# Performance work log

Hardware: AMD Instinct MI355X
Metric: run time of the kernel (lower is better)

## Reference

```python
import jax, jax.numpy as jnp
import numpy as np

N_JOINTS = 24

def _rodrigues(r):
    # r: [B, J, 3] axis-angle -> [B, J, 3, 3] rotation matrices
    theta = jnp.clip(jnp.linalg.norm(r, axis=-1, keepdims=True), 1e-6)  # [B,J,1]
    rh = r / theta
    z = jnp.zeros_like(rh[..., :1])
    # skew-symmetric matrix m
    m = jnp.stack([
        jnp.concatenate([z, -rh[..., 2:3], rh[..., 1:2]], -1),
        jnp.concatenate([rh[..., 2:3], z, -rh[..., 0:1]], -1),
        jnp.concatenate([-rh[..., 1:2], rh[..., 0:1], z], -1),
    ], axis=-2)  # [B,J,3,3]
    rrT = rh[..., :, None] * rh[..., None, :]  # outer product [B,J,3,3]
    cos = jnp.cos(theta)[..., None]
    sin = jnp.sin(theta)[..., None]
    eye = jnp.eye(3, dtype=r.dtype)
    return cos * eye + (1.0 - cos) * rrT + sin * m

def _with_zeros(Rm, t):
    # Rm: [B,3,3], t: [B,3] -> [B,4,4] homogeneous transform
    B = Rm.shape[0]
    top = jnp.concatenate([Rm, t[:, :, None]], axis=-1)  # [B,3,4]
    bot = jnp.broadcast_to(jnp.array([0.0, 0.0, 0.0, 1.0], Rm.dtype), (B, 1, 4))
    return jnp.concatenate([top, bot], axis=1)

def _keypoints(v, idx):
    # v: [B,N,3], idx: [G,K] vertex-index groups -> [B,G,3] via (max+min)/2
    g = v[:, idx]  # [B,G,K,3] irregular gather
    return (g.max(axis=2) + g.min(axis=2)) * 0.5

def setup_inputs() -> dict:
    key = jax.random.key(0)
    ks = jax.random.split(key, 8)
    B, N, P, K = 64, 40000, 100, 128
    beta = jax.random.normal(ks[0], (B, P), jnp.float32)
    pose = jax.random.normal(ks[1], (B, N_JOINTS * 3), jnp.float32) * 0.3
    trans = jax.random.normal(ks[2], (B, 3), jnp.float32)
    shapedirs = jax.random.normal(ks[3], (P, 3 * N), jnp.float32) * 0.01
    v_template = jax.random.normal(ks[4], (N, 3), jnp.float32)
    w = jax.random.uniform(ks[5], (N, N_JOINTS), jnp.float32)
    weights = w / w.sum(axis=1, keepdims=True)  # LBS weights sum to 1
    reorder_index = jnp.arange(N_JOINTS, dtype=jnp.int64 if jax.config.jax_enable_x64 else jnp.int32)
    # kinematic tree: parent[i] < i (binary-tree shape stands in for the rabbit skeleton)
    parent = jnp.concatenate([jnp.zeros(1, jnp.int32), (jnp.arange(1, N_JOINTS, dtype=jnp.int32) - 1) // 2])
    joint_idx = jax.random.randint(ks[6], (N_JOINTS - 1, K), 0, N)
    add_idx = jax.random.randint(ks[7], (7, K), 0, N)
    return {"beta": beta, "pose": pose, "trans": trans, "shapedirs": shapedirs,
            "v_template": v_template, "weights": weights, "reorder_index": reorder_index,
            "parent": parent, "joint_idx": joint_idx, "add_idx": add_idx}

def reference(beta, pose, trans, shapedirs, v_template, weights,
              reorder_index, parent, joint_idx, add_idx):
    B = beta.shape[0]
    pose = pose.reshape(B, N_JOINTS, 3)[:, reorder_index]
    # blend shapes: v_shaped = beta @ shapedirs + template
    v_posed = (beta @ shapedirs + v_template.reshape(-1)).reshape(B, -1, 3)  # [B,N,3]
    # joints from vertex-group (max+min)/2, root is zero
    J = jnp.concatenate([jnp.zeros((B, 1, 3), beta.dtype), _keypoints(v_posed, joint_idx)], axis=1)  # [B,24,3]
    R = _rodrigues(pose)  # [B,24,3,3]
    # forward kinematics along the tree (fixed 24-joint loop)
    par = np.asarray(jax.device_get(parent))
    G = [_with_zeros(R[:, 0], J[:, 0])]
    for i in range(1, N_JOINTS):
        p = int(par[i])
        G_loc = _with_zeros(R[:, i], J[:, i] - J[:, p])
        G.append(jnp.matmul(G[p], G_loc))
    G = jnp.stack(G, axis=1)  # [B,24,4,4]
    # remove rest-pose joint locations (pack subtraction only touches last column)
    Jh = jnp.concatenate([J, jnp.zeros((B, N_JOINTS, 1), beta.dtype)], axis=-1)[..., None]  # [B,24,4,1]
    t_corr = jnp.matmul(G, Jh)  # [B,24,4,1]
    G1 = jnp.concatenate([G[..., :3], G[..., 3:4] - t_corr], axis=-1)
    # LBS skinning: per-vertex blended transform
    T = jnp.einsum('nk,bkij->bnij', weights, G1)  # [B,N,4,4]
    vh = jnp.concatenate([v_posed, jnp.ones((B, v_posed.shape[1], 1), beta.dtype)], axis=-1)  # [B,N,4]
    posed = jnp.einsum('bnij,bnj->bni', T, vh)[..., :3] + trans[:, None, :]  # [B,N,3]
    skeleton = jnp.concatenate([
        jnp.zeros((B, 1, 3), beta.dtype),
        _keypoints(posed, joint_idx),
        _keypoints(posed, add_idx),
    ], axis=1)  # [B,31,3]
    return posed, skeleton
```

## Files before the change

### kernel.cpp

```cpp
#include <hip/hip_runtime.h>
#include <math.h>

#define B    64
#define NV   40000
#define P    100
#define KG   128
#define NJ   24
#define TVJ  16
#define TVS  32
#define NSK  31
#define NSUB (KG / TVJ)
#define NJS  (23 * NSUB)
#define GATHER_BLK 552

typedef __attribute__((ext_vector_type(8))) short bf16x8;
typedef __attribute__((ext_vector_type(4))) float f32x4;

__device__ __forceinline__ unsigned short rne_bf16(float f) {
  unsigned u = __float_as_uint(f);
  u = (u + 0x7FFFu + ((u >> 16) & 1u)) >> 16;
  return (unsigned short)u;
}

__global__ __launch_bounds__(256)
void k_gather(const float* __restrict__ sd,
              const float* __restrict__ beta,
              const int*   __restrict__ joint_idx,
              unsigned short* __restrict__ sdg,
              unsigned short* __restrict__ G1A,
              unsigned short* __restrict__ beta_bf) {
  if (blockIdx.x < GATHER_BLK) {
    const int tid = blockIdx.x * 256 + threadIdx.x;
    const int js = tid / 768, rem = tid % 768;
    const int n = rem % 48, kg = rem / 48;
    const int j = js >> 3, s = js & 7;
    const int vidx = joint_idx[j * KG + s * TVJ + n / 3];
    const size_t colbase = (size_t)vidx * 3 + (n % 3);
    unsigned pk[4];
#pragma unroll
    for (int h = 0; h < 4; ++h) {
      const int k0 = kg * 8 + 2 * h;
      float f0 = 0.0f, f1 = 0.0f;
      if (k0 < P)     f0 = sd[(size_t)k0 * (3 * NV) + colbase];
      if (k0 + 1 < P) f1 = sd[(size_t)(k0 + 1) * (3 * NV) + colbase];
      pk[h] = (unsigned)rne_bf16(f0) | ((unsigned)rne_bf16(f1) << 16);
    }
    *(uint4*)&sdg[(size_t)js * 6144 + n * 128 + kg * 8] =
        make_uint4(pk[0], pk[1], pk[2], pk[3]);
  } else {
    const int e0 = (blockIdx.x - GATHER_BLK) * 256 + threadIdx.x;
    const uint4 z4 = make_uint4(0, 0, 0, 0);
    for (int i = e0; i < 4096; i += 1024) ((uint4*)G1A)[i] = z4;
    for (int i = e0; i < 64 * 136; i += 1024) {
      const int b = i / 136, k = i - b * 136;
      beta_bf[i] = (k < P) ? rne_bf16(beta[b * P + k]) : (unsigned short)0;
    }
  }
}

__global__ __launch_bounds__(256)
void k_jc(const unsigned short* __restrict__ sdg,
          const unsigned short* __restrict__ beta_bf,
          const float* __restrict__ vt,
          const int*   __restrict__ joint_idx,
          const float* __restrict__ pose,
          const float* __restrict__ trans,
          float*       __restrict__ pmn,
          float*       __restrict__ pmx,
          unsigned short* __restrict__ G1A,
          int*         __restrict__ cnt) {
  const int j = blockIdx.x;
  const int s = blockIdx.y;
  const int js = j * NSUB + s;
  const int t = threadIdx.x;
  const int lane = t & 63, wv = t >> 6;
  const int l15 = lane & 15, qd = lane >> 4;

  __shared__ __align__(16) unsigned char smem[55296];
  unsigned short* beta_s = (unsigned short*)smem;
  unsigned short* sdT_s  = (unsigned short*)(smem + 17408);
  float*          vt_s   = (float*)(smem + 30464);
  int*            idx_s  = (int*)(smem + 30656);
  float*          pos_s  = (float*)smem;
  __shared__ int s_old;

  if (t < TVJ) idx_s[t] = joint_idx[j * KG + s * TVJ + t];
  __syncthreads();

  for (int e = t; e < 1088; e += 256)
    ((uint4*)beta_s)[e] = ((const uint4*)beta_bf)[e];
  for (int e = t; e < 768; e += 256) {
    const int n = e >> 4, kg = e & 15;
    *(uint4*)&sdT_s[n * 136 + kg * 8] =
        *(const uint4*)&sdg[(size_t)js * 6144 + (e << 3)];
  }
  if (t < 48) vt_s[t] = vt[(size_t)idx_s[t / 3] * 3 + (t % 3)];
  __syncthreads();

  bf16x8 af[4];
#pragma unroll
  for (int ks = 0; ks < 4; ++ks)
    af[ks] = *(const bf16x8*)&beta_s[(wv * 16 + l15) * 136 + ks * 32 + qd * 8];
  f32x4 acc[3];
#pragma unroll
  for (int nt = 0; nt < 3; ++nt) acc[nt] = (f32x4){0.f, 0.f, 0.f, 0.f};
#pragma unroll
  for (int ks = 0; ks < 4; ++ks) {
#pragma unroll
    for (int nt = 0; nt < 3; ++nt) {
      const bf16x8 bf = *(const bf16x8*)&sdT_s[(nt * 16 + l15) * 136 + ks * 32 + qd * 8];
      acc[nt] = __builtin_amdgcn_mfma_f32_16x16x32_bf16(af[ks], bf, acc[nt], 0, 0, 0);
    }
  }
  float vtv[3];
#pragma unroll
  for (int nt = 0; nt < 3; ++nt) vtv[nt] = vt_s[nt * 16 + l15];
  __syncthreads();

#pragma unroll
  for (int nt = 0; nt < 3; ++nt) {
    const int n = nt * 16 + l15;
    const int v = n / 3, c = n - 3 * v;
#pragma unroll
    for (int r = 0; r < 4; ++r) {
      const int m = wv * 16 + qd * 4 + r;
      pos_s[m * 68 + v * 4 + c] = acc[nt][r] + vtv[nt];
    }
  }
  __syncthreads();

  if (t < 192) {
    const int b = t / 3, c = t % 3;
    float lo = 1e30f, hi = -1e30f;
#pragma unroll
    for (int v = 0; v < TVJ; ++v) {
      const float val = pos_s[b * 68 + v * 4 + c];
      lo = fminf(lo, val); hi = fmaxf(hi, val);
    }
    pmn[(js * B + b) * 3 + c] = lo;
    pmx[(js * B + b) * 3 + c] = hi;
  }

  __syncthreads();
  if (t == 0) { __threadfence(); s_old = atomicAdd(cnt, 1); }
  __syncthreads();
  if (s_old != NJS - 1) return;
  __threadfence();

  float* Jl_c = (float*)smem;
  float* Gl   = (float*)(smem + 18432);

  for (int e = t; e < 192; e += 256) Jl_c[e] = 0.0f;
  for (int e = t; e < 23 * 192; e += 256) {
    const int jj = e / 192, rem = e - jj * 192;
    float lo = 1e30f, hi = -1e30f;
#pragma unroll
    for (int s2 = 0; s2 < NSUB; ++s2) {
      lo = fminf(lo, pmn[(jj * NSUB + s2) * 192 + rem]);
      hi = fmaxf(hi, pmx[(jj * NSUB + s2) * 192 + rem]);
    }
    const int b = rem / 3, c = rem - b * 3;
    Jl_c[((jj + 1) * 3 + c) * 64 + b] = 0.5f * (lo + hi);
  }
  __syncthreads();

  if (t < 64) {
    const int b = t;
    float px = pose[b * 72 + 0], py = pose[b * 72 + 1], pz = pose[b * 72 + 2];
    float G_[12];
#pragma unroll 1
    for (int i = 0; i < NJ; ++i) {
      float nx = 0.f, ny = 0.f, nz = 0.f;
      if (i < NJ - 1) {
        nx = pose[b * 72 + (i + 1) * 3 + 0];
        ny = pose[b * 72 + (i + 1) * 3 + 1];
        nz = pose[b * 72 + (i + 1) * 3 + 2];
      }
      const float th = fmaxf(sqrtf(px * px + py * py + pz * pz), 1e-6f);
      const float xh = px / th, yh = py / th, zh = pz / th;
      const float cc = cosf(th), ss = sinf(th), oo = 1.0f - cc;
      float R9[9];
      R9[0] = cc + oo * xh * xh;      R9[1] = oo * xh * yh - ss * zh; R9[2] = oo * xh * zh + ss * yh;
      R9[3] = oo * xh * yh + ss * zh; R9[4] = cc + oo * yh * yh;      R9[5] = oo * yh * zh - ss * xh;
      R9[6] = oo * xh * zh - ss * yh; R9[7] = oo * yh * zh + ss * xh; R9[8] = cc + oo * zh * zh;

      const float ji0 = Jl_c[(i * 3 + 0) * 64 + b];
      const float ji1 = Jl_c[(i * 3 + 1) * 64 + b];
      const float ji2 = Jl_c[(i * 3 + 2) * 64 + b];

      if (i == 0) {
#pragma unroll
        for (int r = 0; r < 3; ++r) {
          G_[r * 4 + 0] = R9[r * 3 + 0];
          G_[r * 4 + 1] = R9[r * 3 + 1];
          G_[r * 4 + 2] = R9[r * 3 + 2];
          G_[r * 4 + 3] = 0.0f;
        }
      } else {
        const int p = (i - 1) >> 1;
        const float d0 = ji0 - Jl_c[(p * 3 + 0) * 64 + b];
        const float d1 = ji1 - Jl_c[(p * 3 + 1) * 64 + b];
        const float d2 = ji2 - Jl_c[(p * 3 + 2) * 64 + b];
        float Gn[12];
#pragma unroll
        for (int r = 0; r < 3; ++r) {
          const float g0 = Gl[(b * 12 + p) * 12 + r * 4 + 0];
          const float g1 = Gl[(b * 12 + p) * 12 + r * 4 + 1];
          const float g2 = Gl[(b * 12 + p) * 12 + r * 4 + 2];
          const float g3 = Gl[(b * 12 + p) * 12 + r * 4 + 3];
          Gn[r * 4 + 0] = g0 * R9[0] + g1 * R9[3] + g2 * R9[6];
          Gn[r * 4 + 1] = g0 * R9[1] + g1 * R9[4] + g2 * R9[7];
          Gn[r * 4 + 2] = g0 * R9[2] + g1 * R9[5] + g2 * R9[8];
          Gn[r * 4 + 3] = g0 * d0 + g1 * d1 + g2 * d2 + g3;
        }
#pragma unroll
        for (int e = 0; e < 12; ++e) G_[e] = Gn[e];
      }
      if (i < 12) {
#pragma unroll
        for (int e = 0; e < 12; ++e) Gl[(b * 12 + i) * 12 + e] = G_[e];
      }
#pragma unroll
      for (int r = 0; r < 3; ++r) {
        const float tc = G_[r * 4 + 0] * ji0 + G_[r * 4 + 1] * ji1 + G_[r * 4 + 2] * ji2;
        G1A[b * 512 + (r * 4 + 0) * 32 + i] = rne_bf16(G_[r * 4 + 0]);
        G1A[b * 512 + (r * 4 + 1) * 32 + i] = rne_bf16(G_[r * 4 + 1]);
        G1A[b * 512 + (r * 4 + 2) * 32 + i] = rne_bf16(G_[r * 4 + 2]);
        G1A[b * 512 + (r * 4 + 3) * 32 + i] = rne_bf16(G_[r * 4 + 3] - tc);
      }
      px = nx; py = ny; pz = nz;
    }
  } else if (t >= 192) {
#pragma unroll
    for (int k = 0; k < 3; ++k) {
      const int e = (t - 192) * 3 + k;
      const int b = e / 3, r = e - b * 3;
      G1A[b * 512 + (r * 4 + 3) * 32 + 24] = rne_bf16(trans[b * 3 + r]);
    }
  }
}

__global__ __launch_bounds__(256)
void k_skin(const float* __restrict__ sd,
            const float* __restrict__ vt,
            const float* __restrict__ w,
            const unsigned short* __restrict__ beta_bf,
            const unsigned short* __restrict__ G1A,
            float*       __restrict__ out) {
  const int n0v  = blockIdx.x * TVS;
  const int col0 = n0v * 3;
  const int t  = threadIdx.x;
  const int lane = t & 63, wv = t >> 6;
  const int l15 = lane & 15, q = lane >> 4;

  __shared__ __align__(16) unsigned char smem[46464];
  unsigned short* beta_s = (unsigned short*)smem;
  unsigned short* sdT_s  = (unsigned short*)(smem + 17408);
  unsigned short* wT_s   = (unsigned short*)(smem + 43520);
  float*          vt_s   = (float*)(smem + 46080);
  float*          vhf    = (float*)smem;

  for (int e = t; e < 1088; e += 256)
    ((uint4*)beta_s)[e] = ((const uint4*)beta_bf)[e];
  for (int task = t; task < 1536; task += 256) {
    const int n = task % 96, kg = task / 96;
    unsigned pk[4];
#pragma unroll
    for (int h = 0; h < 4; ++h) {
      const int k0 = kg * 8 + 2 * h;
      float f0 = 0.0f, f1 = 0.0f;
      if (k0 < P)     f0 = sd[(size_t)k0 * (3 * NV) + col0 + n];
      if (k0 + 1 < P) f1 = sd[(size_t)(k0 + 1) * (3 * NV) + col0 + n];
      pk[h] = (unsigned)rne_bf16(f0) | ((unsigned)rne_bf16(f1) << 16);
    }
    *(uint4*)&sdT_s[n * 136 + kg * 8] = make_uint4(pk[0], pk[1], pk[2], pk[3]);
  }
  for (int e = t; e < 1024; e += 256) {
    const int n = e >> 5, k = e & 31;
    float val = (k < NJ) ? w[(n0v + n) * NJ + k] : (k == NJ ? 1.0f : 0.0f);
    wT_s[n * 40 + k] = rne_bf16(val);
  }
  if (t < 96) vt_s[t] = vt[col0 + t];
  __syncthreads();

  bf16x8 af[4];
#pragma unroll
  for (int ks = 0; ks < 4; ++ks)
    af[ks] = *(const bf16x8*)&beta_s[(wv * 16 + l15) * 136 + ks * 32 + q * 8];
  f32x4 acc[6];
#pragma unroll
  for (int nt = 0; nt < 6; ++nt) acc[nt] = (f32x4){0.f, 0.f, 0.f, 0.f};
#pragma unroll
  for (int ks = 0; ks < 4; ++ks) {
#pragma unroll
    for (int nt = 0; nt < 6; ++nt) {
      const bf16x8 bf = *(const bf16x8*)&sdT_s[(nt * 16 + l15) * 136 + ks * 32 + q * 8];
      acc[nt] = __builtin_amdgcn_mfma_f32_16x16x32_bf16(af[ks], bf, acc[nt], 0, 0, 0);
    }
  }
  __syncthreads();

#pragma unroll
  for (int nt = 0; nt < 6; ++nt) {
    const int n = nt * 16 + l15;
    const int v = n / 3, c = n - 3 * v;
    const float vtn = vt_s[n];
#pragma unroll
    for (int r = 0; r < 4; ++r) {
      const int m = wv * 16 + q * 4 + r;
      vhf[m * 128 + v * 4 + c] = acc[nt][r] + vtn;
    }
  }
  __syncthreads();

  const bf16x8 wf0 = *(const bf16x8*)&wT_s[l15 * 40 + q * 8];
  const bf16x8 wf1 = *(const bf16x8*)&wT_s[(16 + l15) * 40 + q * 8];
  const f32x4 zero = (f32x4){0.f, 0.f, 0.f, 0.f};
#pragma unroll 4
  for (int bi = 0; bi < 16; ++bi) {
    const int b = wv * 16 + bi;
    const bf16x8 gf = *(const bf16x8*)&G1A[(size_t)b * 512 + l15 * 32 + q * 8];
    const f32x4 d0 = __builtin_amdgcn_mfma_f32_16x16x32_bf16(gf, wf0, zero, 0, 0, 0);
    const f32x4 d1 = __builtin_amdgcn_mfma_f32_16x16x32_bf16(gf, wf1, zero, 0, 0, 0);
    const float4 vh0 = *(const float4*)&vhf[b * 128 + l15 * 4];
    const float4 vh1 = *(const float4*)&vhf[b * 128 + 64 + l15 * 4];
    if (q < 3) {
      out[(size_t)b * (NV * 3) + col0 + l15 * 3 + q] =
          d0[0] * vh0.x + d0[1] * vh0.y + d0[2] * vh0.z + d0[3];
      out[(size_t)b * (NV * 3) + col0 + 48 + l15 * 3 + q] =
          d1[0] * vh1.x + d1[1] * vh1.y + d1[2] * vh1.z + d1[3];
    }
  }
}

__global__ void k_skel(const float* __restrict__ posed,
                       const int*   __restrict__ joint_idx,
                       const int*   __restrict__ add_idx,
                       float*       __restrict__ skel) {
  const int j = blockIdx.x;
  const int b = blockIdx.y;
  const int t = threadIdx.x;
  const int idx = (j < 23) ? joint_idx[j * KG + t] : add_idx[(j - 23) * KG + t];

  const float* p = posed + (size_t)b * NV * 3 + (size_t)idx * 3;
  float mn[3], mx[3];
#pragma unroll
  for (int c = 0; c < 3; ++c) { mn[c] = p[c]; mx[c] = p[c]; }
#pragma unroll
  for (int off = 32; off > 0; off >>= 1) {
#pragma unroll
    for (int c = 0; c < 3; ++c) {
      mn[c] = fminf(mn[c], __shfl_down(mn[c], off));
      mx[c] = fmaxf(mx[c], __shfl_down(mx[c], off));
    }
  }
  __shared__ float s_mn[2][3], s_mx[2][3];
  const int wave = t >> 6, lane = t & 63;
  if (lane == 0) {
#pragma unroll
    for (int c = 0; c < 3; ++c) { s_mn[wave][c] = mn[c]; s_mx[wave][c] = mx[c]; }
  }
  __syncthreads();
  if (t == 0) {
#pragma unroll
    for (int c = 0; c < 3; ++c) {
      float lo = fminf(s_mn[0][c], s_mn[1][c]);
      float hi = fmaxf(s_mx[0][c], s_mx[1][c]);
      skel[(b * NSK + 1 + j) * 3 + c] = 0.5f * (lo + hi);
      if (j == 0) skel[(b * NSK + 0) * 3 + c] = 0.0f;
    }
  }
}

extern "C" void kernel_launch(void* const* d_in, const int* in_sizes, int n_in,
                              void* d_out, int out_size, void* d_ws, size_t ws_size,
                              hipStream_t stream) {
  const float* beta     = (const float*)d_in[0];
  const float* pose     = (const float*)d_in[1];
  const float* trans    = (const float*)d_in[2];
  const float* sd       = (const float*)d_in[3];
  const float* vt       = (const float*)d_in[4];
  const float* w        = (const float*)d_in[5];
  const int* joint_idx  = (const int*)d_in[8];
  const int* add_idx    = (const int*)d_in[9];

  float* out  = (float*)d_out;
  float* skel = out + (size_t)B * NV * 3;
  unsigned short* G1A     = (unsigned short*)d_ws;
  unsigned short* beta_bf = G1A + B * 512;
  float* pmn = (float*)(beta_bf + B * 136);
  float* pmx = pmn + NJS * B * 3;
  int*   cnt = (int*)(pmx + NJS * B * 3);
  unsigned short* sdg = (unsigned short*)(cnt + 4);

  hipMemsetAsync(cnt, 0, 16, stream);
  k_gather<<<GATHER_BLK + 4, 256, 0, stream>>>(sd, beta, joint_idx,
                                               sdg, G1A, beta_bf);
  k_jc<<<dim3(23, NSUB), 256, 0, stream>>>(sdg, beta_bf, vt, joint_idx,
                                           pose, trans, pmn, pmx, G1A, cnt);
  k_skin<<<NV / TVS, 256, 0, stream>>>(sd, vt, w, beta_bf, G1A, out);
  k_skel<<<dim3(30, B), 128, 0, stream>>>(out, joint_idx, add_idx, skel);
}
```

Before: 178.6 us.

## Materialize blended vertices once and reuse them for joints and skinning

Adds a blend kernel that computes the shape-blended vertex positions for all vertices and batches into a workspace buffer. The joint keypoint kernel then gathers from this buffer instead of redoing a bf16 GEMM on gathered shapedirs, and the skinning kernel reads the buffer instead of recomputing the blendshape GEMM. G1A zeroing moves into the last joint block. This removes the separate gather pass and the duplicated GEMM, but adds a large fp32 intermediate write and read.

```diff
diff --git a/kernel.cpp b/kernel.cpp
--- a/kernel.cpp
+++ b/kernel.cpp
@@ -11,7 +11,6 @@
 #define NSK  31
 #define NSUB (KG / TVJ)
 #define NJS  (23 * NSUB)
-#define GATHER_BLK 552
 
 typedef __attribute__((ext_vector_type(8))) short bf16x8;
 typedef __attribute__((ext_vector_type(4))) float f32x4;
@@ -23,122 +22,119 @@
 }
 
 __global__ __launch_bounds__(256)
-void k_gather(const float* __restrict__ sd,
-              const float* __restrict__ beta,
-              const int*   __restrict__ joint_idx,
-              unsigned short* __restrict__ sdg,
-              unsigned short* __restrict__ G1A,
-              unsigned short* __restrict__ beta_bf) {
-  if (blockIdx.x < GATHER_BLK) {
-    const int tid = blockIdx.x * 256 + threadIdx.x;
-    const int js = tid / 768, rem = tid % 768;
-    const int n = rem % 48, kg = rem / 48;
-    const int j = js >> 3, s = js & 7;
-    const int vidx = joint_idx[j * KG + s * TVJ + n / 3];
-    const size_t colbase = (size_t)vidx * 3 + (n % 3);
+void k_blend(const float* __restrict__ beta,
+             const float* __restrict__ sd,
+             const float* __restrict__ vt,
+             float*       __restrict__ vp) {
+  const int n0v  = blockIdx.x * TVS;
+  const int col0 = n0v * 3;
+  const int t  = threadIdx.x;
+  const int lane = t & 63, wv = t >> 6;
+  const int l15 = lane & 15, q = lane >> 4;
+
+  __shared__ __align__(16) unsigned char smem[43904];
+  unsigned short* beta_s = (unsigned short*)smem;
+  unsigned short* sdT_s  = (unsigned short*)(smem + 17408);
+  float*          vt_s   = (float*)(smem + 43520);
+  float*          vhf2   = (float*)smem;
+
+  for (int e = t; e < 64 * 36; e += 256) {
+    const int m = e / 36, pp = P + e % 36;
+    beta_s[m * 136 + pp] = 0;
+  }
+  for (int e = t; e < 64 * P; e += 256) {
+    const int m = e / P, p = e % P;
+    beta_s[m * 136 + p] = rne_bf16(beta[e]);
+  }
+  for (int task = t; task < 1536; task += 256) {
+    const int n = task % 96, kg = task / 96;
     unsigned pk[4];
 #pragma unroll
     for (int h = 0; h < 4; ++h) {
       const int k0 = kg * 8 + 2 * h;
       float f0 = 0.0f, f1 = 0.0f;
-      if (k0 < P)     f0 = sd[(size_t)k0 * (3 * NV) + colbase];
-      if (k0 + 1 < P) f1 = sd[(size_t)(k0 + 1) * (3 * NV) + colbase];
+      if (k0 < P)     f0 = sd[(size_t)k0 * (3 * NV) + col0 + n];
+      if (k0 + 1 < P) f1 = sd[(size_t)(k0 + 1) * (3 * NV) + col0 + n];
       pk[h] = (unsigned)rne_bf16(f0) | ((unsigned)rne_bf16(f1) << 16);
     }
-    *(uint4*)&sdg[(size_t)js * 6144 + n * 128 + kg * 8] =
-        make_uint4(pk[0], pk[1], pk[2], pk[3]);
-  } else {
-    const int e0 = (blockIdx.x - GATHER_BLK) * 256 + threadIdx.x;
-    const uint4 z4 = make_uint4(0, 0, 0, 0);
-    for (int i = e0; i < 4096; i += 1024) ((uint4*)G1A)[i] = z4;
-    for (int i = e0; i < 64 * 136; i += 1024) {
-      const int b = i / 136, k = i - b * 136;
-      beta_bf[i] = (k < P) ? rne_bf16(beta[b * P + k]) : (unsigned short)0;
-    }
-  }
+    *(uint4*)&sdT_s[n * 136 + kg * 8] = make_uint4(pk[0], pk[1], pk[2], pk[3]);
+  }
+  if (t < 96) vt_s[t] = vt[col0 + t];
+  __syncthreads();
+
+  bf16x8 af[4];
+#pragma unroll
+  for (int ks = 0; ks < 4; ++ks)
+    af[ks] = *(const bf16x8*)&beta_s[(wv * 16 + l15) * 136 + ks * 32 + q * 8];
+  f32x4 acc[6];
+#pragma unroll
+  for (int nt = 0; nt < 6; ++nt) acc[nt] = (f32x4){0.f, 0.f, 0.f, 0.f};
+#pragma unroll
+  for (int ks = 0; ks < 4; ++ks) {
+#pragma unroll
+    for (int nt = 0; nt < 6; ++nt) {
+      const bf16x8 bf = *(const bf16x8*)&sdT_s[(nt * 16 + l15) * 136 + ks * 32 + q * 8];
+      acc[nt] = __builtin_amdgcn_mfma_f32_16x16x32_bf16(af[ks], bf, acc[nt], 0, 0, 0);
+    }
+  }
+  __syncthreads();
+
+#pragma unroll
+  for (int nt = 0; nt < 6; ++nt) {
+    const int n = nt * 16 + l15;
+    const int v = n / 3, c = n - 3 * v;
+    const float vtn = vt_s[n];
+#pragma unroll
+    for (int r = 0; r < 4; ++r) {
+      const int m = wv * 16 + q * 4 + r;
+      vhf2[v * 192 + m * 3 + c] = acc[nt][r] + vtn;
+    }
+  }
+  __syncthreads();
+
+  float* dst = vp + (size_t)n0v * 192;
+  const float4* src = (const float4*)smem;
+  for (int e = t; e < 1536; e += 256) ((float4*)dst)[e] = src[e];
 }
 
 __global__ __launch_bounds__(256)
-void k_jc(const unsigned short* __restrict__ sdg,
-          const unsigned short* __restrict__ beta_bf,
-          const float* __restrict__ vt,
-          const int*   __restrict__ joint_idx,
-          const float* __restrict__ pose,
-          const float* __restrict__ trans,
-          float*       __restrict__ pmn,
-          float*       __restrict__ pmx,
-          unsigned short* __restrict__ G1A,
-          int*         __restrict__ cnt) {
+void k_jkp(const float* __restrict__ vp,
+           const int*   __restrict__ joint_idx,
+           const float* __restrict__ pose,
+           const float* __restrict__ trans,
+           float*       __restrict__ pmn,
+           float*       __restrict__ pmx,
+           unsigned short* __restrict__ G1A,
+           int*         __restrict__ cnt) {
   const int j = blockIdx.x;
   const int s = blockIdx.y;
   const int js = j * NSUB + s;
   const int t = threadIdx.x;
-  const int lane = t & 63, wv = t >> 6;
-  const int l15 = lane & 15, qd = lane >> 4;
 
   __shared__ __align__(16) unsigned char smem[55296];
-  unsigned short* beta_s = (unsigned short*)smem;
-  unsigned short* sdT_s  = (unsigned short*)(smem + 17408);
-  float*          vt_s   = (float*)(smem + 30464);
-  int*            idx_s  = (int*)(smem + 30656);
-  float*          pos_s  = (float*)smem;
+  float* pos_s = (float*)smem;
+  __shared__ int idx_s[TVJ];
   __shared__ int s_old;
 
   if (t < TVJ) idx_s[t] = joint_idx[j * KG + s * TVJ + t];
   __syncthreads();
 
-  for (int e = t; e < 1088; e += 256)
-    ((uint4*)beta_s)[e] = ((const uint4*)beta_bf)[e];
-  for (int e = t; e < 768; e += 256) {
-    const int n = e >> 4, kg = e & 15;
-    *(uint4*)&sdT_s[n * 136 + kg * 8] =
-        *(const uint4*)&sdg[(size_t)js * 6144 + (e << 3)];
-  }
-  if (t < 48) vt_s[t] = vt[(size_t)idx_s[t / 3] * 3 + (t % 3)];
-  __syncthreads();
-
-  bf16x8 af[4];
-#pragma unroll
-  for (int ks = 0; ks < 4; ++ks)
-    af[ks] = *(const bf16x8*)&beta_s[(wv * 16 + l15) * 136 + ks * 32 + qd * 8];
-  f32x4 acc[3];
-#pragma unroll
-  for (int nt = 0; nt < 3; ++nt) acc[nt] = (f32x4){0.f, 0.f, 0.f, 0.f};
-#pragma unroll
-  for (int ks = 0; ks < 4; ++ks) {
-#pragma unroll
-    for (int nt = 0; nt < 3; ++nt) {
-      const bf16x8 bf = *(const bf16x8*)&sdT_s[(nt * 16 + l15) * 136 + ks * 32 + qd * 8];
-      acc[nt] = __builtin_amdgcn_mfma_f32_16x16x32_bf16(af[ks], bf, acc[nt], 0, 0, 0);
-    }
-  }
-  float vtv[3];
-#pragma unroll
-  for (int nt = 0; nt < 3; ++nt) vtv[nt] = vt_s[nt * 16 + l15];
-  __syncthreads();
-
-#pragma unroll
-  for (int nt = 0; nt < 3; ++nt) {
-    const int n = nt * 16 + l15;
-    const int v = n / 3, c = n - 3 * v;
-#pragma unroll
-    for (int r = 0; r < 4; ++r) {
-      const int m = wv * 16 + qd * 4 + r;
-      pos_s[m * 68 + v * 4 + c] = acc[nt][r] + vtv[nt];
-    }
+  for (int task = t; task < 768; task += 256) {
+    const int r = task / 48, c4 = task % 48;
+    const float4 v = *(const float4*)&vp[(size_t)idx_s[r] * 192 + c4 * 4];
+    *(float4*)&pos_s[r * 192 + c4 * 4] = v;
   }
   __syncthreads();
 
   if (t < 192) {
-    const int b = t / 3, c = t % 3;
     float lo = 1e30f, hi = -1e30f;
 #pragma unroll
     for (int v = 0; v < TVJ; ++v) {
-      const float val = pos_s[b * 68 + v * 4 + c];
+      const float val = pos_s[v * 192 + t];
       lo = fminf(lo, val); hi = fmaxf(hi, val);
     }
-    pmn[(js * B + b) * 3 + c] = lo;
-    pmx[(js * B + b) * 3 + c] = hi;
+    pmn[js * 192 + t] = lo;
+    pmx[js * 192 + t] = hi;
   }
 
   __syncthreads();
@@ -150,6 +146,10 @@
   float* Jl_c = (float*)smem;
   float* Gl   = (float*)(smem + 18432);
 
+  {
+    const uint4 z4 = make_uint4(0, 0, 0, 0);
+    for (int e = t; e < 4096; e += 256) ((uint4*)G1A)[e] = z4;
+  }
   for (int e = t; e < 192; e += 256) Jl_c[e] = 0.0f;
   for (int e = t; e < 23 * 192; e += 256) {
     const int jj = e / 192, rem = e - jj * 192;
@@ -241,75 +241,35 @@
 }
 
 __global__ __launch_bounds__(256)
-void k_skin(const float* __restrict__ sd,
-            const float* __restrict__ vt,
-            const float* __restrict__ w,
-            const unsigned short* __restrict__ beta_bf,
-            const unsigned short* __restrict__ G1A,
-            float*       __restrict__ out) {
+void k_skin2(const float* __restrict__ vp,
+             const float* __restrict__ w,
+             const unsigned short* __restrict__ G1A,
+             float*       __restrict__ out) {
   const int n0v  = blockIdx.x * TVS;
   const int col0 = n0v * 3;
   const int t  = threadIdx.x;
   const int lane = t & 63, wv = t >> 6;
   const int l15 = lane & 15, q = lane >> 4;
 
-  __shared__ __align__(16) unsigned char smem[46464];
-  unsigned short* beta_s = (unsigned short*)smem;
-  unsigned short* sdT_s  = (unsigned short*)(smem + 17408);
-  unsigned short* wT_s   = (unsigned short*)(smem + 43520);
-  float*          vt_s   = (float*)(smem + 46080);
-  float*          vhf    = (float*)smem;
-
-  for (int e = t; e < 1088; e += 256)
-    ((uint4*)beta_s)[e] = ((const uint4*)beta_bf)[e];
-  for (int task = t; task < 1536; task += 256) {
-    const int n = task % 96, kg = task / 96;
-    unsigned pk[4];
-#pragma unroll
-    for (int h = 0; h < 4; ++h) {
-      const int k0 = kg * 8 + 2 * h;
-      float f0 = 0.0f, f1 = 0.0f;
-      if (k0 < P)     f0 = sd[(size_t)k0 * (3 * NV) + col0 + n];
-      if (k0 + 1 < P) f1 = sd[(size_t)(k0 + 1) * (3 * NV) + col0 + n];
-      pk[h] = (unsigned)rne_bf16(f0) | ((unsigned)rne_bf16(f1) << 16);
-    }
-    *(uint4*)&sdT_s[n * 136 + kg * 8] = make_uint4(pk[0], pk[1], pk[2], pk[3]);
+  __shared__ __align__(16) unsigned char smem[35328];
+  float*          vhf  = (float*)smem;
+  unsigned short* wT_s = (unsigned short*)(smem + 32768);
+
+  for (int e = t; e < 1536; e += 256) {
+    const int v = e / 48, j0 = (e % 48) * 4;
+    const float4 f = *(const float4*)&vp[(size_t)(n0v + v) * 192 + j0];
+    const float ff[4] = {f.x, f.y, f.z, f.w};
+#pragma unroll
+    for (int i = 0; i < 4; ++i) {
+      const int jj = j0 + i;
+      const int m = jj / 3, c = jj - 3 * m;
+      vhf[m * 128 + v * 4 + c] = ff[i];
+    }
   }
   for (int e = t; e < 1024; e += 256) {
     const int n = e >> 5, k = e & 31;
     float val = (k < NJ) ? w[(n0v + n) * NJ + k] : (k == NJ ? 1.0f : 0.0f);
     wT_s[n * 40 + k] = rne_bf16(val);
-  }
-  if (t < 96) vt_s[t] = vt[col0 + t];
-  __syncthreads();
-
-  bf16x8 af[4];
-#pragma unroll
-  for (int ks = 0; ks < 4; ++ks)
-    af[ks] = *(const bf16x8*)&beta_s[(wv * 16 + l15) * 136 + ks * 32 + q * 8];
-  f32x4 acc[6];
-#pragma unroll
-  for (int nt = 0; nt < 6; ++nt) acc[nt] = (f32x4){0.f, 0.f, 0.f, 0.f};
-#pragma unroll
-  for (int ks = 0; ks < 4; ++ks) {
-#pragma unroll
-    for (int nt = 0; nt < 6; ++nt) {
-      const bf16x8 bf = *(const bf16x8*)&sdT_s[(nt * 16 + l15) * 136 + ks * 32 + q * 8];
-      acc[nt] = __builtin_amdgcn_mfma_f32_16x16x32_bf16(af[ks], bf, acc[nt], 0, 0, 0);
-    }
-  }
-  __syncthreads();
-
-#pragma unroll
-  for (int nt = 0; nt < 6; ++nt) {
-    const int n = nt * 16 + l15;
-    const int v = n / 3, c = n - 3 * v;
-    const float vtn = vt_s[n];
-#pragma unroll
-    for (int r = 0; r < 4; ++r) {
-      const int m = wv * 16 + q * 4 + r;
-      vhf[m * 128 + v * 4 + c] = acc[nt][r] + vtn;
-    }
   }
   __syncthreads();
 
@@ -386,18 +346,16 @@
 
   float* out  = (float*)d_out;
   float* skel = out + (size_t)B * NV * 3;
-  unsigned short* G1A     = (unsigned short*)d_ws;
-  unsigned short* beta_bf = G1A + B * 512;
-  float* pmn = (float*)(beta_bf + B * 136);
-  float* pmx = pmn + NJS * B * 3;
-  int*   cnt = (int*)(pmx + NJS * B * 3);
-  unsigned short* sdg = (unsigned short*)(cnt + 4);
+  unsigned short* G1A = (unsigned short*)d_ws;
+  float* pmn = (float*)((char*)d_ws + 65536);
+  float* pmx = (float*)((char*)d_ws + 206848);
+  int*   cnt = (int*)((char*)d_ws + 348160);
+  float* vp  = (float*)((char*)d_ws + 348176);
 
   hipMemsetAsync(cnt, 0, 16, stream);
-  k_gather<<<GATHER_BLK + 4, 256, 0, stream>>>(sd, beta, joint_idx,
-                                               sdg, G1A, beta_bf);
-  k_jc<<<dim3(23, NSUB), 256, 0, stream>>>(sdg, beta_bf, vt, joint_idx,
-                                           pose, trans, pmn, pmx, G1A, cnt);
-  k_skin<<<NV / TVS, 256, 0, stream>>>(sd, vt, w, beta_bf, G1A, out);
+  k_blend<<<NV / TVS, 256, 0, stream>>>(beta, sd, vt, vp);
+  k_jkp<<<dim3(23, NSUB), 256, 0, stream>>>(vp, joint_idx, pose, trans,
+                                            pmn, pmx, G1A, cnt);
+  k_skin2<<<NV / TVS, 256, 0, stream>>>(vp, w, G1A, out);
   k_skel<<<dim3(30, B), 128, 0, stream>>>(out, joint_idx, add_idx, skel);
 }
```

Result: slower. 183.3 us (+2.6%).

## Bucket joint indices by vertex tile and reduce joint bounds with atomics

Applied to the files above, without the earlier changes.

The per-joint gather of shapedirs columns is replaced. Joint vertex indices are now bucketed by 16-vertex tile, and each tile block blends its contiguous vertices with MFMA and folds min/max into per-joint bounds using order-preserving integer atomics. The forward-kinematics chain moves into its own single-block kernel, which drops the last-block counter. The LBS weights are also converted to padded bf16 once up front, so the skinning kernel can load them as vectors. In exchange the code adds launches and reads many whole tiles instead of only the gathered columns. A fixed bucket capacity of 16 would silently drop indices if a tile ever overflowed.

```diff
diff --git a/kernel.cpp b/kernel.cpp
--- a/kernel.cpp
+++ b/kernel.cpp
@@ -6,12 +6,11 @@
 #define P    100
 #define KG   128
 #define NJ   24
-#define TVJ  16
+#define TVB  16
 #define TVS  32
 #define NSK  31
-#define NSUB (KG / TVJ)
-#define NJS  (23 * NSUB)
-#define GATHER_BLK 552
+#define NTIL (NV / TVB)
+#define BCAP 16
 
 typedef __attribute__((ext_vector_type(8))) short bf16x8;
 typedef __attribute__((ext_vector_type(4))) float f32x4;
@@ -21,86 +20,101 @@
   u = (u + 0x7FFFu + ((u >> 16) & 1u)) >> 16;
   return (unsigned short)u;
 }
+__device__ __forceinline__ unsigned fkey(float f) {
+  const unsigned u = __float_as_uint(f);
+  return (u & 0x80000000u) ? ~u : (u | 0x80000000u);
+}
+__device__ __forceinline__ float unfkey(unsigned k) {
+  const unsigned u = (k & 0x80000000u) ? (k ^ 0x80000000u) : ~k;
+  return __uint_as_float(u);
+}
 
 __global__ __launch_bounds__(256)
-void k_gather(const float* __restrict__ sd,
-              const float* __restrict__ beta,
-              const int*   __restrict__ joint_idx,
-              unsigned short* __restrict__ sdg,
-              unsigned short* __restrict__ G1A,
-              unsigned short* __restrict__ beta_bf) {
-  if (blockIdx.x < GATHER_BLK) {
-    const int tid = blockIdx.x * 256 + threadIdx.x;
-    const int js = tid / 768, rem = tid % 768;
-    const int n = rem % 48, kg = rem / 48;
-    const int j = js >> 3, s = js & 7;
-    const int vidx = joint_idx[j * KG + s * TVJ + n / 3];
-    const size_t colbase = (size_t)vidx * 3 + (n % 3);
+void k_prep0(const float* __restrict__ beta,
+             const float* __restrict__ w,
+             unsigned short* __restrict__ beta_bf,
+             unsigned short* __restrict__ wbf,
+             unsigned short* __restrict__ G1A,
+             unsigned* __restrict__ pmnU,
+             unsigned* __restrict__ pmxU,
+             int* __restrict__ tileCnt) {
+  const int tid  = blockIdx.x * 256 + threadIdx.x;
+  const int nthr = gridDim.x * 256;
+  const uint4 z4 = make_uint4(0, 0, 0, 0);
+  for (int e = tid; e < 4096; e += nthr) ((uint4*)G1A)[e] = z4;
+  for (int e = tid; e < 23 * 192; e += nthr) { pmnU[e] = 0xFFFFFFFFu; pmxU[e] = 0u; }
+  for (int e = tid; e < NTIL; e += nthr) tileCnt[e] = 0;
+  for (int e = tid; e < 64 * 136; e += nthr) {
+    const int b = e / 136, k = e - b * 136;
+    beta_bf[e] = (k < P) ? rne_bf16(beta[b * P + k]) : (unsigned short)0;
+  }
+  for (int e = tid; e < NV * 32; e += nthr) {
+    const int n = e >> 5, k = e & 31;
+    const float val = (k < NJ) ? w[n * NJ + k] : (k == NJ ? 1.0f : 0.0f);
+    wbf[e] = rne_bf16(val);
+  }
+}
+
+__global__ __launch_bounds__(256)
+void k_prep1(const int* __restrict__ joint_idx,
+             int* __restrict__ tileCnt,
+             unsigned* __restrict__ tileBuck) {
+  const int e = blockIdx.x * 256 + threadIdx.x;
+  if (e >= 23 * KG) return;
+  const int j = e >> 7;
+  const int vidx = joint_idx[e];
+  const int tile = vidx >> 4;
+  const int slot = atomicAdd(&tileCnt[tile], 1);
+  if (slot < BCAP)
+    tileBuck[tile * BCAP + slot] = ((unsigned)j << 16) | (unsigned)vidx;
+}
+
+__global__ __launch_bounds__(256)
+void k_blendJ(const unsigned short* __restrict__ beta_bf,
+              const float* __restrict__ sd,
+              const float* __restrict__ vt,
+              const int* __restrict__ tileCnt,
+              const unsigned* __restrict__ tileBuck,
+              unsigned* __restrict__ pmnU,
+              unsigned* __restrict__ pmxU) {
+  const int bid  = blockIdx.x;
+  const int hc0  = tileCnt[bid];
+  if (hc0 == 0) return;
+  const int hc   = (hc0 < BCAP) ? hc0 : BCAP;
+  const int n0v  = bid * TVB;
+  const int col0 = n0v * 3;
+  const int t  = threadIdx.x;
+  const int lane = t & 63, wv = t >> 6;
+  const int l15 = lane & 15, q = lane >> 4;
+
+  __shared__ __align__(16) unsigned char smem[30656];
+  unsigned short* beta_s = (unsigned short*)smem;
+  unsigned short* sdT_s  = (unsigned short*)(smem + 17408);
+  float*          vt_s   = (float*)(smem + 30464);
+  float*          pos_s  = (float*)smem;
+
+  for (int e = t; e < 1088; e += 256)
+    ((uint4*)beta_s)[e] = ((const uint4*)beta_bf)[e];
+  for (int task = t; task < 768; task += 256) {
+    const int n = task % 48, kg = task / 48;
     unsigned pk[4];
 #pragma unroll
     for (int h = 0; h < 4; ++h) {
       const int k0 = kg * 8 + 2 * h;
       float f0 = 0.0f, f1 = 0.0f;
-      if (k0 < P)     f0 = sd[(size_t)k0 * (3 * NV) + colbase];
-      if (k0 + 1 < P) f1 = sd[(size_t)(k0 + 1) * (3 * NV) + colbase];
+      if (k0 < P)     f0 = sd[(size_t)k0 * (3 * NV) + col0 + n];
+      if (k0 + 1 < P) f1 = sd[(size_t)(k0 + 1) * (3 * NV) + col0 + n];
       pk[h] = (unsigned)rne_bf16(f0) | ((unsigned)rne_bf16(f1) << 16);
     }
-    *(uint4*)&sdg[(size_t)js * 6144 + n * 128 + kg * 8] =
-        make_uint4(pk[0], pk[1], pk[2], pk[3]);
-  } else {
-    const int e0 = (blockIdx.x - GATHER_BLK) * 256 + threadIdx.x;
-    const uint4 z4 = make_uint4(0, 0, 0, 0);
-    for (int i = e0; i < 4096; i += 1024) ((uint4*)G1A)[i] = z4;
-    for (int i = e0; i < 64 * 136; i += 1024) {
-      const int b = i / 136, k = i - b * 136;
-      beta_bf[i] = (k < P) ? rne_bf16(beta[b * P + k]) : (unsigned short)0;
-    }
-  }
-}
-
-__global__ __launch_bounds__(256)
-void k_jc(const unsigned short* __restrict__ sdg,
-          const unsigned short* __restrict__ beta_bf,
-          const float* __restrict__ vt,
-          const int*   __restrict__ joint_idx,
-          const float* __restrict__ pose,
-          const float* __restrict__ trans,
-          float*       __restrict__ pmn,
-          float*       __restrict__ pmx,
-          unsigned short* __restrict__ G1A,
-          int*         __restrict__ cnt) {
-  const int j = blockIdx.x;
-  const int s = blockIdx.y;
-  const int js = j * NSUB + s;
-  const int t = threadIdx.x;
-  const int lane = t & 63, wv = t >> 6;
-  const int l15 = lane & 15, qd = lane >> 4;
-
-  __shared__ __align__(16) unsigned char smem[55296];
-  unsigned short* beta_s = (unsigned short*)smem;
-  unsigned short* sdT_s  = (unsigned short*)(smem + 17408);
-  float*          vt_s   = (float*)(smem + 30464);
-  int*            idx_s  = (int*)(smem + 30656);
-  float*          pos_s  = (float*)smem;
-  __shared__ int s_old;
-
-  if (t < TVJ) idx_s[t] = joint_idx[j * KG + s * TVJ + t];
-  __syncthreads();
-
-  for (int e = t; e < 1088; e += 256)
-    ((uint4*)beta_s)[e] = ((const uint4*)beta_bf)[e];
-  for (int e = t; e < 768; e += 256) {
-    const int n = e >> 4, kg = e & 15;
-    *(uint4*)&sdT_s[n * 136 + kg * 8] =
-        *(const uint4*)&sdg[(size_t)js * 6144 + (e << 3)];
-  }
-  if (t < 48) vt_s[t] = vt[(size_t)idx_s[t / 3] * 3 + (t % 3)];
+    *(uint4*)&sdT_s[n * 136 + kg * 8] = make_uint4(pk[0], pk[1], pk[2], pk[3]);
+  }
+  if (t < 48) vt_s[t] = vt[col0 + t];
   __syncthreads();
 
   bf16x8 af[4];
 #pragma unroll
   for (int ks = 0; ks < 4; ++ks)
-    af[ks] = *(const bf16x8*)&beta_s[(wv * 16 + l15) * 136 + ks * 32 + qd * 8];
+    af[ks] = *(const bf16x8*)&beta_s[(wv * 16 + l15) * 136 + ks * 32 + q * 8];
   f32x4 acc[3];
 #pragma unroll
   for (int nt = 0; nt < 3; ++nt) acc[nt] = (f32x4){0.f, 0.f, 0.f, 0.f};
@@ -108,7 +122,7 @@
   for (int ks = 0; ks < 4; ++ks) {
 #pragma unroll
     for (int nt = 0; nt < 3; ++nt) {
-      const bf16x8 bf = *(const bf16x8*)&sdT_s[(nt * 16 + l15) * 136 + ks * 32 + qd * 8];
+      const bf16x8 bf = *(const bf16x8*)&sdT_s[(nt * 16 + l15) * 136 + ks * 32 + q * 8];
       acc[nt] = __builtin_amdgcn_mfma_f32_16x16x32_bf16(af[ks], bf, acc[nt], 0, 0, 0);
     }
   }
@@ -123,42 +137,41 @@
     const int v = n / 3, c = n - 3 * v;
 #pragma unroll
     for (int r = 0; r < 4; ++r) {
-      const int m = wv * 16 + qd * 4 + r;
+      const int m = wv * 16 + q * 4 + r;
       pos_s[m * 68 + v * 4 + c] = acc[nt][r] + vtv[nt];
     }
   }
   __syncthreads();
 
-  if (t < 192) {
-    const int b = t / 3, c = t % 3;
-    float lo = 1e30f, hi = -1e30f;
-#pragma unroll
-    for (int v = 0; v < TVJ; ++v) {
-      const float val = pos_s[b * 68 + v * 4 + c];
-      lo = fminf(lo, val); hi = fmaxf(hi, val);
-    }
-    pmn[(js * B + b) * 3 + c] = lo;
-    pmx[(js * B + b) * 3 + c] = hi;
-  }
-
-  __syncthreads();
-  if (t == 0) { __threadfence(); s_old = atomicAdd(cnt, 1); }
-  __syncthreads();
-  if (s_old != NJS - 1) return;
-  __threadfence();
-
+  for (int k = 0; k < hc; ++k) {
+    const unsigned e = tileBuck[bid * BCAP + k];
+    const int j = (int)(e >> 16);
+    const int v = (int)(e & 0xFFFFu) - n0v;
+    if (t < 192) {
+      const int b = t / 3, c = t - 3 * (t / 3);
+      const unsigned key = fkey(pos_s[b * 68 + v * 4 + c]);
+      atomicMin(&pmnU[j * 192 + t], key);
+      atomicMax(&pmxU[j * 192 + t], key);
+    }
+  }
+}
+
+__global__ __launch_bounds__(256)
+void k_chain(const unsigned* __restrict__ pmnU,
+             const unsigned* __restrict__ pmxU,
+             const float* __restrict__ pose,
+             const float* __restrict__ trans,
+             unsigned short* __restrict__ G1A) {
+  const int t = threadIdx.x;
+  __shared__ __align__(16) unsigned char smem[55296];
   float* Jl_c = (float*)smem;
   float* Gl   = (float*)(smem + 18432);
 
   for (int e = t; e < 192; e += 256) Jl_c[e] = 0.0f;
   for (int e = t; e < 23 * 192; e += 256) {
     const int jj = e / 192, rem = e - jj * 192;
-    float lo = 1e30f, hi = -1e30f;
-#pragma unroll
-    for (int s2 = 0; s2 < NSUB; ++s2) {
-      lo = fminf(lo, pmn[(jj * NSUB + s2) * 192 + rem]);
-      hi = fmaxf(hi, pmx[(jj * NSUB + s2) * 192 + rem]);
-    }
+    const float lo = unfkey(pmnU[e]);
+    const float hi = unfkey(pmxU[e]);
     const int b = rem / 3, c = rem - b * 3;
     Jl_c[((jj + 1) * 3 + c) * 64 + b] = 0.5f * (lo + hi);
   }
@@ -243,7 +256,7 @@
 __global__ __launch_bounds__(256)
 void k_skin(const float* __restrict__ sd,
             const float* __restrict__ vt,
-            const float* __restrict__ w,
+            const unsigned short* __restrict__ wbf,
             const unsigned short* __restrict__ beta_bf,
             const unsigned short* __restrict__ G1A,
             float*       __restrict__ out) {
@@ -275,10 +288,10 @@
     }
     *(uint4*)&sdT_s[n * 136 + kg * 8] = make_uint4(pk[0], pk[1], pk[2], pk[3]);
   }
-  for (int e = t; e < 1024; e += 256) {
-    const int n = e >> 5, k = e & 31;
-    float val = (k < NJ) ? w[(n0v + n) * NJ + k] : (k == NJ ? 1.0f : 0.0f);
-    wT_s[n * 40 + k] = rne_bf16(val);
+  for (int e = t; e < 128; e += 256) {
+    const int n = e >> 2, kg = e & 3;
+    *(uint4*)&wT_s[n * 40 + kg * 8] =
+        ((const uint4*)wbf)[(size_t)(n0v + n) * 4 + kg];
   }
   if (t < 96) vt_s[t] = vt[col0 + t];
   __syncthreads();
@@ -386,18 +399,20 @@
 
   float* out  = (float*)d_out;
   float* skel = out + (size_t)B * NV * 3;
-  unsigned short* G1A     = (unsigned short*)d_ws;
-  unsigned short* beta_bf = G1A + B * 512;
-  float* pmn = (float*)(beta_bf + B * 136);
-  float* pmx = pmn + NJS * B * 3;
-  int*   cnt = (int*)(pmx + NJS * B * 3);
-  unsigned short* sdg = (unsigned short*)(cnt + 4);
-
-  hipMemsetAsync(cnt, 0, 16, stream);
-  k_gather<<<GATHER_BLK + 4, 256, 0, stream>>>(sd, beta, joint_idx,
-                                               sdg, G1A, beta_bf);
-  k_jc<<<dim3(23, NSUB), 256, 0, stream>>>(sdg, beta_bf, vt, joint_idx,
-                                           pose, trans, pmn, pmx, G1A, cnt);
-  k_skin<<<NV / TVS, 256, 0, stream>>>(sd, vt, w, beta_bf, G1A, out);
+  unsigned short* G1A      = (unsigned short*)d_ws;
+  unsigned* pmnU           = (unsigned*)((char*)d_ws + 65536);
+  unsigned* pmxU           = (unsigned*)((char*)d_ws + 83200);
+  int*      tileCnt        = (int*)((char*)d_ws + 100864);
+  unsigned* tileBuck       = (unsigned*)((char*)d_ws + 110864);
+  unsigned short* beta_bf  = (unsigned short*)((char*)d_ws + 270864);
+  unsigned short* wbf      = (unsigned short*)((char*)d_ws + 288272);
+
+  k_prep0<<<512, 256, 0, stream>>>(beta, w, beta_bf, wbf, G1A,
+                                   pmnU, pmxU, tileCnt);
+  k_prep1<<<12, 256, 0, stream>>>(joint_idx, tileCnt, tileBuck);
+  k_blendJ<<<NTIL, 256, 0, stream>>>(beta_bf, sd, vt, tileCnt, tileBuck,
+                                     pmnU, pmxU);
+  k_chain<<<1, 256, 0, stream>>>(pmnU, pmxU, pose, trans, G1A);
+  k_skin<<<NV / TVS, 256, 0, stream>>>(sd, vt, wbf, beta_bf, G1A, out);
   k_skel<<<dim3(30, B), 128, 0, stream>>>(out, joint_idx, add_idx, skel);
 }
```

Result: no change. 178.3 us (-0.2%).
